# Kernel optimization log

Hardware: AMD Instinct MI355X
Metric: run time of the kernel (lower is better)

## Reference

```python
import jax, jax.numpy as jnp
import numpy as np

INPUT_SIZE = 32
HIDDEN_SIZE = 64
OUTPUT_SIZE = 8
B, T = 8192, 128


def setup_inputs() -> dict:
    key = jax.random.key(0)
    ks = jax.random.split(key, 7)
    s_ih = 1.0 / np.sqrt(HIDDEN_SIZE)
    return {
        "x": jax.random.normal(ks[0], (B, T, INPUT_SIZE), dtype=jnp.float32),
        "W_ih": jax.random.uniform(ks[1], (4 * HIDDEN_SIZE, INPUT_SIZE), minval=-s_ih, maxval=s_ih),
        "W_hh": jax.random.uniform(ks[2], (4 * HIDDEN_SIZE, HIDDEN_SIZE), minval=-s_ih, maxval=s_ih),
        "b_ih": jax.random.uniform(ks[3], (4 * HIDDEN_SIZE,), minval=-s_ih, maxval=s_ih),
        "b_hh": jax.random.uniform(ks[4], (4 * HIDDEN_SIZE,), minval=-s_ih, maxval=s_ih),
        "W_fc": jax.random.uniform(ks[5], (OUTPUT_SIZE, HIDDEN_SIZE), minval=-s_ih, maxval=s_ih),
        "b_fc": jax.random.uniform(ks[6], (OUTPUT_SIZE,), minval=-s_ih, maxval=s_ih),
    }


def _lstm_last_h(x, W_ih, W_hh, b_ih, b_hh):
    Bc, Tc, _ = x.shape
    H = HIDDEN_SIZE
    # Precompute the input contribution to all gates once: [B, T, 4H]
    x_gates = jnp.einsum("bti,gi->btg", x, W_ih) + b_ih + b_hh

    def step(carry, xg_t):  # xg_t: [B, 4H]
        h, c = carry
        gates = xg_t + h @ W_hh.T
        i = jax.nn.sigmoid(gates[:, 0 * H:1 * H])
        f = jax.nn.sigmoid(gates[:, 1 * H:2 * H])
        g = jnp.tanh(gates[:, 2 * H:3 * H])
        o = jax.nn.sigmoid(gates[:, 3 * H:4 * H])
        c = f * c + i * g
        h = o * jnp.tanh(c)
        return (h, c), None

    h0 = jnp.zeros((Bc, H), dtype=x.dtype)
    c0 = jnp.zeros((Bc, H), dtype=x.dtype)
    (h_T, _), _ = jax.lax.scan(step, (h0, c0), jnp.swapaxes(x_gates, 0, 1))
    return h_T  # [B, H] = out[:, -1, :]


def reference(x, W_ih, W_hh, b_ih, b_hh, W_fc, b_fc):
    h_last = _lstm_last_h(x, W_ih, W_hh, b_ih, b_hh)
    return h_last @ W_fc.T + b_fc  # [B, OUTPUT_SIZE]
```

## Files before the change

### kernel.cpp

```cpp
#include <hip/hip_runtime.h>
#include <stdint.h>


#define T_STEPS 128
#define ISZ 32
#define HSZ 64
#define B_TOT 8192
#define B_TILE 16
#define T_CHUNK 32
#define HPAD 144

typedef short bf16x8 __attribute__((ext_vector_type(8)));
typedef float f32x4 __attribute__((ext_vector_type(4)));

#define LOG2E 1.44269504088896340736f

__device__ __forceinline__ float bf2f(unsigned short s) {
    union { unsigned int u; float f; } v; v.u = ((unsigned int)s) << 16; return v.f;
}
__device__ __forceinline__ unsigned short f2bf(float f) {
    union { float f; unsigned int u; } v; v.f = f;
    unsigned int u = v.u;
    return (unsigned short)((u + 0x7fffu + ((u >> 16) & 1u)) >> 16);
}
__device__ __forceinline__ float sigf(float x) {
    return __builtin_amdgcn_rcpf(1.0f + __builtin_amdgcn_exp2f(-LOG2E * x));
}
__device__ __forceinline__ float tanh_fast(float x) {
    return 1.0f - 2.0f * __builtin_amdgcn_rcpf(1.0f + __builtin_amdgcn_exp2f((2.0f * LOG2E) * x));
}

template <bool F32>
__device__ __forceinline__ float ldin(const void* p, size_t i) {
    if (F32) return ((const float*)p)[i];
    return bf2f(((const unsigned short*)p)[i]);
}

template <bool F32>
__device__ __forceinline__ void run_body(
    const void* xv, const void* Wihv, const void* Whhv, const void* bihv,
    const void* bhhv, const void* Wfcv, const void* bfcv, void* outv,
    unsigned short (&hbuf)[2][B_TILE][HPAD],
    unsigned short (&xbuf)[T_CHUNK][B_TILE][40],
    float (&hfin)[B_TILE][HSZ + 4])
{
    const int tid  = threadIdx.x;
    const int wid  = tid >> 6;
    const int lane = tid & 63;
    const int q    = lane >> 4;
    const int tn   = lane & 15;
    const int u    = wid * 16 + tn;
    const int b0   = blockIdx.x * B_TILE;

    bf16x8 wf[4][3];
    float bias[4];
    #pragma unroll
    for (int g = 0; g < 4; ++g) {
        const int row = g * HSZ + u;
        #pragma unroll
        for (int j = 0; j < 8; ++j) {
            wf[g][0][j] = (short)f2bf(ldin<F32>(Whhv, row * HSZ + q * 8 + j));
            wf[g][1][j] = (short)f2bf(ldin<F32>(Whhv, row * HSZ + 32 + q * 8 + j));
            wf[g][2][j] = (short)f2bf(ldin<F32>(Wihv, row * ISZ + q * 8 + j));
        }
        bias[g] = ldin<F32>(bihv, row) + ldin<F32>(bhhv, row);
    }

    for (int i = tid; i < 2 * B_TILE * HPAD; i += 256) ((unsigned short*)hbuf)[i] = 0;

    float cst[4] = {0.f, 0.f, 0.f, 0.f};
    float hl[4]  = {0.f, 0.f, 0.f, 0.f};

    for (int tc = 0; tc < T_STEPS / T_CHUNK; ++tc) {
        if (F32) {
            const float* xf = (const float*)xv;
            for (int idx = tid; idx < B_TILE * T_CHUNK * 4; idx += 256) {
                const int m  = idx >> 7;
                const int rm = idx & 127;
                const int tl = rm >> 2;
                const int ch = rm & 3;
                const size_t base = ((size_t)(b0 + m) * T_STEPS + (tc * T_CHUNK + tl)) * ISZ + ch * 8;
                const f32x4 v0 = *(const f32x4*)(xf + base);
                const f32x4 v1 = *(const f32x4*)(xf + base + 4);
                bf16x8 w;
                #pragma unroll
                for (int j = 0; j < 4; ++j) {
                    w[j]     = (short)f2bf(v0[j]);
                    w[4 + j] = (short)f2bf(v1[j]);
                }
                *(bf16x8*)&xbuf[tl][m][ch * 8] = w;
            }
        } else {
            const unsigned short* xu = (const unsigned short*)xv;
            for (int idx = tid; idx < B_TILE * T_CHUNK * 4; idx += 256) {
                const int m  = idx >> 7;
                const int rm = idx & 127;
                const int tl = rm >> 2;
                const int ch = rm & 3;
                const uint4 v = *(const uint4*)(xu + ((size_t)(b0 + m) * T_STEPS + (tc * T_CHUNK + tl)) * ISZ + ch * 8);
                *(uint4*)&xbuf[tl][m][ch * 8] = v;
            }
        }
        __syncthreads();

        #pragma unroll 2
        for (int tl = 0; tl < T_CHUNK; ++tl) {
            const int t  = tc * T_CHUNK + tl;
            const int rb = t & 1, wb = rb ^ 1;
            const bf16x8 a0 = *(const bf16x8*)&hbuf[rb][tn][q * 8];
            const bf16x8 a1 = *(const bf16x8*)&hbuf[rb][tn][32 + q * 8];
            const bf16x8 ax = *(const bf16x8*)&xbuf[tl][tn][q * 8];

            f32x4 acc[4];
            #pragma unroll
            for (int g = 0; g < 4; ++g) {
                #pragma unroll
                for (int e = 0; e < 4; ++e) acc[g][e] = bias[g];
                acc[g] = __builtin_amdgcn_mfma_f32_16x16x32_bf16(a0, wf[g][0], acc[g], 0, 0, 0);
                acc[g] = __builtin_amdgcn_mfma_f32_16x16x32_bf16(a1, wf[g][1], acc[g], 0, 0, 0);
                acc[g] = __builtin_amdgcn_mfma_f32_16x16x32_bf16(ax, wf[g][2], acc[g], 0, 0, 0);
            }
            #pragma unroll
            for (int r = 0; r < 4; ++r) {
                const float gi = sigf(acc[0][r]);
                const float gf = sigf(acc[1][r]);
                const float gg = tanh_fast(acc[2][r]);
                const float go = sigf(acc[3][r]);
                cst[r] = gf * cst[r] + gi * gg;
                const float hv = go * tanh_fast(cst[r]);
                hl[r] = hv;
                const int m = q * 4 + r;
                hbuf[wb][m][u] = f2bf(hv);
            }
            __syncthreads();
        }
    }

    #pragma unroll
    for (int r = 0; r < 4; ++r) hfin[q * 4 + r][u] = hl[r];
    __syncthreads();
    if (tid < B_TILE * 8) {
        const int m = tid >> 3, j = tid & 7;
        float s = ldin<F32>(bfcv, j);
        #pragma unroll
        for (int k = 0; k < HSZ; ++k) s += hfin[m][k] * ldin<F32>(Wfcv, j * HSZ + k);
        const size_t o = (size_t)(b0 + m) * 8 + j;
        if (F32) ((float*)outv)[o] = s;
        else     ((unsigned short*)outv)[o] = f2bf(s);
    }
}

__global__ __launch_bounds__(256, 2) void lstm_fused(
    const void* __restrict__ x, const void* __restrict__ Wih,
    const void* __restrict__ Whh, const void* __restrict__ bih,
    const void* __restrict__ bhh, const void* __restrict__ Wfc,
    const void* __restrict__ bfc, void* __restrict__ out)
{
    __shared__ unsigned short hbuf[2][B_TILE][HPAD];
    __shared__ unsigned short xbuf[T_CHUNK][B_TILE][40];
    __shared__ float hfin[B_TILE][HSZ + 4];

    const unsigned short* xu = (const unsigned short*)x;
    const int lane = threadIdx.x & 63;
    const unsigned short s0 = xu[lane * 2];
    const unsigned short s1 = xu[lane * 2 + 1];
    const int big = (((s0 >> 7) & 0xFF) >= 0x90) || (((s1 >> 7) & 0xFF) >= 0x90);
    const bool isf32 = __any(big) != 0;

    if (isf32) run_body<true >(x, Wih, Whh, bih, bhh, Wfc, bfc, out, hbuf, xbuf, hfin);
    else       run_body<false>(x, Wih, Whh, bih, bhh, Wfc, bfc, out, hbuf, xbuf, hfin);
}

extern "C" void kernel_launch(void* const* d_in, const int* in_sizes, int n_in,
                              void* d_out, int out_size, void* d_ws, size_t ws_size,
                              hipStream_t stream) {
    lstm_fused<<<dim3(B_TOT / B_TILE), dim3(256), 0, stream>>>(
        d_in[0], d_in[1], d_in[2], d_in[3], d_in[4], d_in[5], d_in[6], d_out);
}
```

Baseline: 279.6 us.

## Double threads per block and split gate activations across two wave groups

The block grows from 4 to 8 waves. Each pair of waves computes the same MFMA gate tiles redundantly, and each wave then applies the sigmoid/tanh elementwise work to only half of the accumulator rows. This halves the per-wave transcendental work on the serial recurrence critical path, at the cost of duplicated MFMA work, more register pressure under the raised launch bounds (NTHR, 4), and a block-wide barrier across more waves each step.

```diff
diff --git a/kernel.cpp b/kernel.cpp
--- a/kernel.cpp
+++ b/kernel.cpp
@@ -9,6 +9,7 @@
 #define B_TILE 16
 #define T_CHUNK 32
 #define HPAD 144
+#define NTHR 512
 
 typedef short bf16x8 __attribute__((ext_vector_type(8)));
 typedef float f32x4 __attribute__((ext_vector_type(4)));
@@ -49,7 +50,9 @@
     const int lane = tid & 63;
     const int q    = lane >> 4;
     const int tn   = lane & 15;
-    const int u    = wid * 16 + tn;
+    const int ug   = wid & 3;
+    const int rh   = wid >> 2;
+    const int u    = ug * 16 + tn;
     const int b0   = blockIdx.x * B_TILE;
 
     bf16x8 wf[4][3];
@@ -66,15 +69,15 @@
         bias[g] = ldin<F32>(bihv, row) + ldin<F32>(bhhv, row);
     }
 
-    for (int i = tid; i < 2 * B_TILE * HPAD; i += 256) ((unsigned short*)hbuf)[i] = 0;
+    for (int i = tid; i < 2 * B_TILE * HPAD; i += NTHR) ((unsigned short*)hbuf)[i] = 0;
 
-    float cst[4] = {0.f, 0.f, 0.f, 0.f};
-    float hl[4]  = {0.f, 0.f, 0.f, 0.f};
+    float cst[2] = {0.f, 0.f};
+    float hl[2]  = {0.f, 0.f};
 
     for (int tc = 0; tc < T_STEPS / T_CHUNK; ++tc) {
         if (F32) {
             const float* xf = (const float*)xv;
-            for (int idx = tid; idx < B_TILE * T_CHUNK * 4; idx += 256) {
+            for (int idx = tid; idx < B_TILE * T_CHUNK * 4; idx += NTHR) {
                 const int m  = idx >> 7;
                 const int rm = idx & 127;
                 const int tl = rm >> 2;
@@ -92,7 +95,7 @@
             }
         } else {
             const unsigned short* xu = (const unsigned short*)xv;
-            for (int idx = tid; idx < B_TILE * T_CHUNK * 4; idx += 256) {
+            for (int idx = tid; idx < B_TILE * T_CHUNK * 4; idx += NTHR) {
                 const int m  = idx >> 7;
                 const int rm = idx & 127;
                 const int tl = rm >> 2;
@@ -121,14 +124,15 @@
                 acc[g] = __builtin_amdgcn_mfma_f32_16x16x32_bf16(ax, wf[g][2], acc[g], 0, 0, 0);
             }
             #pragma unroll
-            for (int r = 0; r < 4; ++r) {
+            for (int rr = 0; rr < 2; ++rr) {
+                const int r  = rh * 2 + rr;
                 const float gi = sigf(acc[0][r]);
                 const float gf = sigf(acc[1][r]);
                 const float gg = tanh_fast(acc[2][r]);
                 const float go = sigf(acc[3][r]);
-                cst[r] = gf * cst[r] + gi * gg;
-                const float hv = go * tanh_fast(cst[r]);
-                hl[r] = hv;
+                cst[rr] = gf * cst[rr] + gi * gg;
+                const float hv = go * tanh_fast(cst[rr]);
+                hl[rr] = hv;
                 const int m = q * 4 + r;
                 hbuf[wb][m][u] = f2bf(hv);
             }
@@ -137,7 +141,7 @@
     }
 
     #pragma unroll
-    for (int r = 0; r < 4; ++r) hfin[q * 4 + r][u] = hl[r];
+    for (int rr = 0; rr < 2; ++rr) hfin[q * 4 + rh * 2 + rr][u] = hl[rr];
     __syncthreads();
     if (tid < B_TILE * 8) {
         const int m = tid >> 3, j = tid & 7;
@@ -150,7 +154,7 @@
     }
 }
 
-__global__ __launch_bounds__(256, 2) void lstm_fused(
+__global__ __launch_bounds__(NTHR, 4) void lstm_fused(
     const void* __restrict__ x, const void* __restrict__ Wih,
     const void* __restrict__ Whh, const void* __restrict__ bih,
     const void* __restrict__ bhh, const void* __restrict__ Wfc,
@@ -174,6 +178,6 @@
 extern "C" void kernel_launch(void* const* d_in, const int* in_sizes, int n_in,
                               void* d_out, int out_size, void* d_ws, size_t ws_size,
                               hipStream_t stream) {
-    lstm_fused<<<dim3(B_TOT / B_TILE), dim3(256), 0, stream>>>(
+    lstm_fused<<<dim3(B_TOT / B_TILE), dim3(NTHR), 0, stream>>>(
         d_in[0], d_in[1], d_in[2], d_in[3], d_in[4], d_in[5], d_in[6], d_out);
 }
```

Result: slower. 308.0 us (+10.1%).
